# Kernel tuning notes

Hardware: AMD Instinct MI355X
Metric: run time of the kernel (lower is better)

The kernel has to match this reference:

```python
import jax, jax.numpy as jnp
import numpy as np

E = 8          # num_experts
K = 2          # experts_per_token
D = 1024       # d_model
F = 2048       # dim_feedforward
B, S = 2, 2048

def setup_inputs() -> dict:
    key = jax.random.key(0)
    ks = jax.random.split(key, 5)
    scale = 0.02
    return {
        "x":   jax.random.normal(ks[0], (B, S, D), jnp.float32),
        "Wr":  jax.random.normal(ks[1], (E, D), jnp.float32) * scale,
        "temp": jnp.ones((1,), jnp.float32),
        "W1":  jax.random.normal(ks[2], (E, 2 * F, D), jnp.float32) * scale,
        "b1":  jnp.zeros((E, 2 * F), jnp.float32),
        "W2":  jax.random.normal(ks[3], (E, D, F), jnp.float32) * scale,
        "b2":  jnp.zeros((E, D), jnp.float32),
    }

def reference(x, Wr, temp, W1, b1, W2, b2):
    b, s, d = x.shape
    xf = x.reshape(-1, d)                                   # [T, D]
    router_logits = (xf @ Wr.T) / temp                      # [T, E]
    # eval mode: no router noise, dropout is identity
    top_w, top_idx = jax.lax.top_k(router_logits, K)        # [T, K]
    top_w = jax.nn.softmax(top_w, axis=-1)                  # renormalize over top-k
    # dense gate matrix [T, E]: weight if expert selected else 0 (topk indices are distinct)
    gates = jnp.sum(jax.nn.one_hot(top_idx, E, dtype=xf.dtype) * top_w[..., None], axis=1)
    out = jnp.zeros_like(xf)
    for e in range(E):  # fixed small expert loop, dense compute gated to zero for unrouted tokens
        h = xf @ W1[e].T + b1[e]                            # [T, 2F]
        a = h[:, :F] * jax.nn.silu(h[:, F:])                # SwiGLU -> [T, F]
        y = a @ W2[e].T + b2[e]                             # [T, D]
        out = out + y * gates[:, e:e + 1]
    return out.reshape(b, s, d)
```

## Files before the change

### kernel.cpp

```cpp
#include <hip/hip_runtime.h>
#include <hip/hip_bf16.h>

#define DEV __device__ __forceinline__

namespace {

constexpr int D     = 1024;
constexpr int F     = 2048;
constexpr int E     = 8;
constexpr int TWO_F = 2 * F;

typedef short bf16x8 __attribute__((ext_vector_type(8)));
typedef float f32x4  __attribute__((ext_vector_type(4)));

DEV unsigned short f32_to_bf16(float f) {
  unsigned int u = __builtin_bit_cast(unsigned int, f);
  u += 0x7fffu + ((u >> 16) & 1u);
  return (unsigned short)(u >> 16);
}

DEV void load_lds16(const void* g, void* l) {
  __builtin_amdgcn_global_load_lds((const __attribute__((address_space(1))) void*)g,
                                   (__attribute__((address_space(3))) void*)l, 16, 0, 0);
}

DEV const bf16x8* frag_addr(const unsigned short* S, int row, int kk, int quad) {
  int cl = (((kk >> 3) + quad) ^ (row & 7));
  return (const bf16x8*)(S + row * 64 + cl * 8);
}

__global__ void zero_kernel(float* __restrict__ p, int n4) {
  int i = blockIdx.x * 256 + threadIdx.x;
  if (i < n4) ((float4*)p)[i] = make_float4(0.f, 0.f, 0.f, 0.f);
}

__global__ void cvt_all_kernel(const float* __restrict__ x, const float* __restrict__ W1,
                               const float* __restrict__ W2,
                               unsigned short* __restrict__ xb, unsigned short* __restrict__ W1b,
                               unsigned short* __restrict__ W2b,
                               long long nx, long long n1) {
  long long i = (long long)(blockIdx.x * 256 + threadIdx.x) * 8;
  const float* src;
  unsigned short* dst;
  long long off;
  if (i < nx)            { src = x;  dst = xb;  off = i; }
  else if (i < nx + n1)  { src = W1; dst = W1b; off = i - nx; }
  else                   { src = W2; dst = W2b; off = i - nx - n1; }
  float4 a = *(const float4*)(src + off);
  float4 b = *(const float4*)(src + off + 4);
  uint4 o;
  o.x = (unsigned)f32_to_bf16(a.x) | ((unsigned)f32_to_bf16(a.y) << 16);
  o.y = (unsigned)f32_to_bf16(a.z) | ((unsigned)f32_to_bf16(a.w) << 16);
  o.z = (unsigned)f32_to_bf16(b.x) | ((unsigned)f32_to_bf16(b.y) << 16);
  o.w = (unsigned)f32_to_bf16(b.z) | ((unsigned)f32_to_bf16(b.w) << 16);
  *(uint4*)(dst + off) = o;
}

__global__ void router_kernel(const float* __restrict__ x, const float* __restrict__ Wr,
                              const float* __restrict__ temp,
                              int* __restrict__ topk_idx, float* __restrict__ topk_gate, int T) {
  int wid  = blockIdx.x * 4 + (threadIdx.x >> 6);
  int lane = threadIdx.x & 63;
  if (wid >= T) return;
  const float* xr = x + (size_t)wid * D;
  float acc[E];
#pragma unroll
  for (int e = 0; e < E; ++e) acc[e] = 0.f;
  int base = lane * 16;
#pragma unroll
  for (int u = 0; u < 4; ++u) {
    float4 xv = *(const float4*)(xr + base + u * 4);
#pragma unroll
    for (int e = 0; e < E; ++e) {
      float4 wv = *(const float4*)(Wr + e * D + base + u * 4);
      acc[e] += xv.x * wv.x + xv.y * wv.y + xv.z * wv.z + xv.w * wv.w;
    }
  }
#pragma unroll
  for (int e = 0; e < E; ++e) {
    float v = acc[e];
#pragma unroll
    for (int off = 32; off > 0; off >>= 1) v += __shfl_xor(v, off, 64);
    acc[e] = v;
  }
  if (lane == 0) {
    float inv = 1.0f / temp[0];
    float l[E];
#pragma unroll
    for (int e = 0; e < E; ++e) l[e] = acc[e] * inv;
    int e0 = 0;
#pragma unroll
    for (int e = 1; e < E; ++e) if (l[e] > l[e0]) e0 = e;
    int e1 = (e0 == 0) ? 1 : 0;
#pragma unroll
    for (int e = 0; e < E; ++e) if (e != e0 && l[e] > l[e1]) e1 = e;
    float dlt = l[e1] - l[e0];
    float ed  = __expf(dlt);
    topk_idx[2 * wid]      = e0;
    topk_idx[2 * wid + 1]  = e1;
    topk_gate[2 * wid]     = 1.f / (1.f + ed);
    topk_gate[2 * wid + 1] = ed / (1.f + ed);
  }
}

__global__ __launch_bounds__(1024)
void assign_kernel(const int* __restrict__ topk_idx, const float* __restrict__ topk_gate,
                   int* __restrict__ counts, int* __restrict__ offsets,
                   int* __restrict__ row_token, float* __restrict__ row_gate, int T) {
  __shared__ int hist[E];
  __shared__ int cur[E];
  const int tid = threadIdx.x;
  if (tid < E) hist[tid] = 0;
  __syncthreads();
  for (int t = tid; t < T; t += 1024) {
    atomicAdd(&hist[topk_idx[2 * t]], 1);
    atomicAdd(&hist[topk_idx[2 * t + 1]], 1);
  }
  __syncthreads();
  if (tid == 0) {
    int s = 0;
    for (int e = 0; e < E; ++e) {
      int c = hist[e];
      counts[e]  = c;
      offsets[e] = s;
      cur[e]     = s;
      s += c;
    }
  }
  __syncthreads();
  for (int t = tid; t < T; t += 1024) {
#pragma unroll
    for (int s = 0; s < 2; ++s) {
      int e = topk_idx[2 * t + s];
      int p = atomicAdd(&cur[e], 1);
      row_token[p] = t;
      row_gate[p]  = topk_gate[2 * t + s];
    }
  }
}

__global__ __launch_bounds__(256, 2)
void gemm1_kernel(const unsigned short* __restrict__ xb,
                  const unsigned short* __restrict__ W1b,
                  const float* __restrict__ b1,
                  const int* __restrict__ counts, const int* __restrict__ offsets,
                  const int* __restrict__ row_token,
                  unsigned short* __restrict__ a_buf) {
  const int e  = blockIdx.z;
  const int m0 = blockIdx.y * 128;
  const int n0 = blockIdx.x * 64;
  const int cnt = counts[e];
  if (m0 >= cnt) return;
  const int pairBase = offsets[e];

  __shared__ __align__(16) unsigned short As[128 * 64];
  __shared__ __align__(16) unsigned short Bs[128 * 64];
  __shared__ int tokS[128];

  const int tid = threadIdx.x;
  if (tid < 128) {
    int r = m0 + tid;
    tokS[tid] = (r < cnt) ? row_token[pairBase + r] : row_token[pairBase];
  }
  __syncthreads();

  const int lane = tid & 63;
  const int wave = tid >> 6;
  const int quad = lane >> 4;
  const int l16  = lane & 15;
  const int lr   = lane >> 3;
  const int lc   = lane & 7;
  const int sw   = lc ^ (lr & 7);
  const int wr   = wave >> 1;
  const int wc   = wave & 1;

  const unsigned short* W1e = W1b + (size_t)e * TWO_F * D;
  const unsigned short* aptr[4];
  const unsigned short* bptr[4];
#pragma unroll
  for (int i = 0; i < 4; ++i) {
    int r = wave * 32 + i * 8 + lr;
    aptr[i] = xb + (size_t)tokS[r] * D + sw * 8;
    int g = r >> 5, s = r & 31;
    int wrow = (g & 1) * F + n0 + (g >> 1) * 32 + s;
    bptr[i] = W1e + (size_t)wrow * D + sw * 8;
  }
  unsigned short* AsW = As + (wave * 32) * 64;
  unsigned short* BsW = Bs + (wave * 32) * 64;

  f32x4 acc[4][4];
#pragma unroll
  for (int i = 0; i < 4; ++i)
#pragma unroll
    for (int j = 0; j < 4; ++j) acc[i][j] = (f32x4){0.f, 0.f, 0.f, 0.f};

  for (int k0 = 0; k0 < D; k0 += 64) {
#pragma unroll
    for (int i = 0; i < 4; ++i) load_lds16(aptr[i] + k0, AsW + i * 8 * 64);
#pragma unroll
    for (int i = 0; i < 4; ++i) load_lds16(bptr[i] + k0, BsW + i * 8 * 64);
    __syncthreads();
#pragma unroll
    for (int kk = 0; kk < 64; kk += 32) {
      bf16x8 af[4], bf[4];
#pragma unroll
      for (int i = 0; i < 4; ++i)
        af[i] = *frag_addr(As, wr * 64 + i * 16 + l16, kk, quad);
#pragma unroll
      for (int j = 0; j < 4; ++j)
        bf[j] = *frag_addr(Bs, wc * 64 + j * 16 + l16, kk, quad);
#pragma unroll
      for (int i = 0; i < 4; ++i)
#pragma unroll
        for (int j = 0; j < 4; ++j)
          acc[i][j] = __builtin_amdgcn_mfma_f32_16x16x32_bf16(af[i], bf[j], acc[i][j], 0, 0, 0);
    }
    __syncthreads();
  }

#pragma unroll
  for (int i = 0; i < 4; ++i) {
    int rb = wr * 64 + i * 16 + quad * 4;
#pragma unroll
    for (int j = 0; j < 2; ++j) {
      int col = n0 + wc * 32 + j * 16 + l16;
      float bh1 = b1[e * TWO_F + col];
      float bh2 = b1[e * TWO_F + F + col];
#pragma unroll
      for (int rg = 0; rg < 4; ++rg) {
        int r = rb + rg;
        if (m0 + r < cnt) {
          float h1 = acc[i][j][rg] + bh1;
          float h2 = acc[i][j + 2][rg] + bh2;
          float a  = h1 * (h2 / (1.f + __expf(-h2)));
          a_buf[(size_t)(pairBase + m0 + r) * F + col] = f32_to_bf16(a);
        }
      }
    }
  }
}

__global__ __launch_bounds__(256, 2)
void gemm2_kernel(const unsigned short* __restrict__ a_buf,
                  const unsigned short* __restrict__ W2b,
                  const float* __restrict__ b2,
                  const int* __restrict__ counts, const int* __restrict__ offsets,
                  const int* __restrict__ row_token, const float* __restrict__ row_gate,
                  float* __restrict__ out, int totalPairs) {
  const int e  = blockIdx.z;
  const int m0 = blockIdx.y * 128;
  const int n0 = blockIdx.x * 128;
  const int cnt = counts[e];
  if (m0 >= cnt) return;
  const int pairBase = offsets[e];

  __shared__ __align__(16) unsigned short As[128 * 64];
  __shared__ __align__(16) unsigned short Bs[128 * 64];
  __shared__ int   tokS[128];
  __shared__ float gateS[128];

  const int tid = threadIdx.x;
  if (tid < 128) {
    int r = m0 + tid;
    bool v = (r < cnt);
    tokS[tid]  = v ? row_token[pairBase + r] : 0;
    gateS[tid] = v ? row_gate[pairBase + r] : 0.f;
  }
  __syncthreads();

  const int lane = tid & 63;
  const int wave = tid >> 6;
  const int quad = lane >> 4;
  const int l16  = lane & 15;
  const int lr   = lane >> 3;
  const int lc   = lane & 7;
  const int sw   = lc ^ (lr & 7);
  const int wr   = wave >> 1;
  const int wc   = wave & 1;

  const unsigned short* W2e = W2b + (size_t)e * D * F;
  const unsigned short* aptr[4];
  const unsigned short* bptr[4];
#pragma unroll
  for (int i = 0; i < 4; ++i) {
    int r = wave * 32 + i * 8 + lr;
    int g = pairBase + m0 + r;
    if (g > totalPairs - 1) g = totalPairs - 1;
    aptr[i] = a_buf + (size_t)g * F + sw * 8;
    bptr[i] = W2e + (size_t)(n0 + r) * F + sw * 8;
  }
  unsigned short* AsW = As + (wave * 32) * 64;
  unsigned short* BsW = Bs + (wave * 32) * 64;

  f32x4 acc[4][4];
#pragma unroll
  for (int i = 0; i < 4; ++i)
#pragma unroll
    for (int j = 0; j < 4; ++j) acc[i][j] = (f32x4){0.f, 0.f, 0.f, 0.f};

  for (int k0 = 0; k0 < F; k0 += 64) {
#pragma unroll
    for (int i = 0; i < 4; ++i) load_lds16(aptr[i] + k0, AsW + i * 8 * 64);
#pragma unroll
    for (int i = 0; i < 4; ++i) load_lds16(bptr[i] + k0, BsW + i * 8 * 64);
    __syncthreads();
#pragma unroll
    for (int kk = 0; kk < 64; kk += 32) {
      bf16x8 af[4], bf[4];
#pragma unroll
      for (int i = 0; i < 4; ++i)
        af[i] = *frag_addr(As, wr * 64 + i * 16 + l16, kk, quad);
#pragma unroll
      for (int j = 0; j < 4; ++j)
        bf[j] = *frag_addr(Bs, wc * 64 + j * 16 + l16, kk, quad);
#pragma unroll
      for (int i = 0; i < 4; ++i)
#pragma unroll
        for (int j = 0; j < 4; ++j)
          acc[i][j] = __builtin_amdgcn_mfma_f32_16x16x32_bf16(af[i], bf[j], acc[i][j], 0, 0, 0);
    }
    __syncthreads();
  }

#pragma unroll
  for (int j = 0; j < 4; ++j) {
    int col = n0 + wc * 64 + j * 16 + l16;
    float b2v = b2[e * D + col];
#pragma unroll
    for (int i = 0; i < 4; ++i) {
      int rb = wr * 64 + i * 16 + quad * 4;
#pragma unroll
      for (int rg = 0; rg < 4; ++rg) {
        int r = rb + rg;
        if (m0 + r < cnt) {
          float y = (acc[i][j][rg] + b2v) * gateS[r];
          atomicAdd(&out[(size_t)tokS[r] * D + col], y);
        }
      }
    }
  }
}

}

extern "C" void kernel_launch(void* const* d_in, const int* in_sizes, int n_in,
                              void* d_out, int out_size, void* d_ws, size_t ws_size,
                              hipStream_t stream) {
  (void)n_in; (void)out_size; (void)ws_size;
  const float* x    = (const float*)d_in[0];
  const float* Wr   = (const float*)d_in[1];
  const float* temp = (const float*)d_in[2];
  const float* W1   = (const float*)d_in[3];
  const float* b1   = (const float*)d_in[4];
  const float* W2   = (const float*)d_in[5];
  const float* b2   = (const float*)d_in[6];
  float* out = (float*)d_out;
  const int T = in_sizes[0] / D;

  char* ws = (char*)d_ws;
  size_t off = 0;
  unsigned short* xb    = (unsigned short*)(ws + off); off += (size_t)T * D * 2;
  unsigned short* W1b   = (unsigned short*)(ws + off); off += (size_t)E * TWO_F * D * 2;
  unsigned short* W2b   = (unsigned short*)(ws + off); off += (size_t)E * D * F * 2;
  unsigned short* a_buf = (unsigned short*)(ws + off); off += (size_t)T * 2 * F * 2;
  int*   counts    = (int*)(ws + off); off += 64;
  int*   offsets   = (int*)(ws + off); off += 64;
  int*   topk_idx  = (int*)(ws + off); off += (size_t)T * 2 * 4;
  float* topk_gate = (float*)(ws + off); off += (size_t)T * 2 * 4;
  int*   row_token = (int*)(ws + off); off += (size_t)T * 2 * 4;
  float* row_gate  = (float*)(ws + off); off += (size_t)T * 2 * 4;

  const long long nx = (long long)T * D;
  const long long n1 = (long long)E * TWO_F * D;
  const long long n2 = (long long)E * D * F;

  zero_kernel<<<(T * D / 4 + 255) / 256, 256, 0, stream>>>(out, T * D / 4);
  router_kernel<<<(T + 3) / 4, 256, 0, stream>>>(x, Wr, temp, topk_idx, topk_gate, T);
  assign_kernel<<<1, 1024, 0, stream>>>(topk_idx, topk_gate, counts, offsets,
                                        row_token, row_gate, T);
  cvt_all_kernel<<<(int)((nx + n1 + n2) / 2048), 256, 0, stream>>>(x, W1, W2, xb, W1b, W2b,
                                                                   nx, n1);
  gemm1_kernel<<<dim3(F / 64, (T * 2 + 127) / 128, E), 256, 0, stream>>>(xb, W1b, b1, counts,
                                                                         offsets, row_token, a_buf);
  gemm2_kernel<<<dim3(D / 128, (T * 2 + 127) / 128, E), 256, 0, stream>>>(a_buf, W2b, b2, counts,
                                                                          offsets, row_token,
                                                                          row_gate, out, T * 2);
}
```

Measured before the change: 476.6 us.

## Replace atomic scatter-add with bf16 expert output buffer and gather combine

Removes the zero kernel and the float atomicAdd scatter in gemm2. gemm2 now writes bf16 per-pair outputs into a buffer that reuses the W1b workspace, and a new combine kernel gathers each token's two expert rows and applies the gate weights. The assign kernel now uses deterministic ballot/popcount ranking instead of shared atomics and records each pair's position. Launch bounds on both GEMMs are raised to 4 blocks per CU. Costs are an extra launch, an extra bf16 round trip for expert outputs, and possible register pressure from the higher occupancy target.

```diff
diff --git a/kernel.cpp b/kernel.cpp
--- a/kernel.cpp
+++ b/kernel.cpp
@@ -19,6 +19,11 @@
   return (unsigned short)(u >> 16);
 }
 
+DEV float bf16_to_f32(unsigned short h) {
+  unsigned int u = ((unsigned int)h) << 16;
+  return __builtin_bit_cast(float, u);
+}
+
 DEV void load_lds16(const void* g, void* l) {
   __builtin_amdgcn_global_load_lds((const __attribute__((address_space(1))) void*)g,
                                    (__attribute__((address_space(3))) void*)l, 16, 0, 0);
@@ -27,11 +32,6 @@
 DEV const bf16x8* frag_addr(const unsigned short* S, int row, int kk, int quad) {
   int cl = (((kk >> 3) + quad) ^ (row & 7));
   return (const bf16x8*)(S + row * 64 + cl * 8);
-}
-
-__global__ void zero_kernel(float* __restrict__ p, int n4) {
-  int i = blockIdx.x * 256 + threadIdx.x;
-  if (i < n4) ((float4*)p)[i] = make_float4(0.f, 0.f, 0.f, 0.f);
 }
 
 __global__ void cvt_all_kernel(const float* __restrict__ x, const float* __restrict__ W1,
@@ -105,41 +105,65 @@
 
 __global__ __launch_bounds__(1024)
 void assign_kernel(const int* __restrict__ topk_idx, const float* __restrict__ topk_gate,
-                   int* __restrict__ counts, int* __restrict__ offsets,
-                   int* __restrict__ row_token, float* __restrict__ row_gate, int T) {
-  __shared__ int hist[E];
-  __shared__ int cur[E];
-  const int tid = threadIdx.x;
-  if (tid < E) hist[tid] = 0;
+                   int* __restrict__ counts, int* __restrict__ offsets_g,
+                   int* __restrict__ row_token, float* __restrict__ row_gate,
+                   int* __restrict__ pos, int T) {
+  __shared__ int cntS[128 * E];
+  __shared__ int baseS[128 * E];
+  __shared__ int totS[E];
+  __shared__ int offS[E];
+  const int tid  = threadIdx.x;
+  const int w    = tid >> 6;
+  const int lane = tid & 63;
+  const int Q    = 2 * T;
+  const unsigned long long lm = (1ull << lane) - 1ull;
+
+  int eReg[8], rReg[8];
+#pragma unroll
+  for (int c = 0; c < 8; ++c) {
+    int q = (w * 8 + c) * 64 + lane;
+    int e = (q < Q) ? topk_idx[q] : -1;
+    eReg[c] = e;
+    int r = 0;
+#pragma unroll
+    for (int ee = 0; ee < E; ++ee) {
+      unsigned long long m = __ballot(e == ee);
+      if (lane == ee) cntS[(w * 8 + c) * E + ee] = __popcll(m);
+      if (e == ee) r = __popcll(m & lm);
+    }
+    rReg[c] = r;
+  }
   __syncthreads();
-  for (int t = tid; t < T; t += 1024) {
-    atomicAdd(&hist[topk_idx[2 * t]], 1);
-    atomicAdd(&hist[topk_idx[2 * t + 1]], 1);
+  if (tid < E) {
+    int s = 0;
+    for (int k = 0; k < 128; ++k) { baseS[k * E + tid] = s; s += cntS[k * E + tid]; }
+    totS[tid] = s;
   }
   __syncthreads();
   if (tid == 0) {
     int s = 0;
     for (int e = 0; e < E; ++e) {
-      int c = hist[e];
-      counts[e]  = c;
-      offsets[e] = s;
-      cur[e]     = s;
-      s += c;
+      offS[e] = s;
+      counts[e] = totS[e];
+      offsets_g[e] = s;
+      s += totS[e];
     }
   }
   __syncthreads();
-  for (int t = tid; t < T; t += 1024) {
-#pragma unroll
-    for (int s = 0; s < 2; ++s) {
-      int e = topk_idx[2 * t + s];
-      int p = atomicAdd(&cur[e], 1);
-      row_token[p] = t;
-      row_gate[p]  = topk_gate[2 * t + s];
-    }
-  }
-}
-
-__global__ __launch_bounds__(256, 2)
+#pragma unroll
+  for (int c = 0; c < 8; ++c) {
+    int q = (w * 8 + c) * 64 + lane;
+    if (q < Q) {
+      int e = eReg[c];
+      int p = offS[e] + baseS[(w * 8 + c) * E + e] + rReg[c];
+      row_token[p] = q >> 1;
+      row_gate[p]  = topk_gate[q];
+      pos[q]       = p;
+    }
+  }
+}
+
+__global__ __launch_bounds__(256, 4)
 void gemm1_kernel(const unsigned short* __restrict__ xb,
                   const unsigned short* __restrict__ W1b,
                   const float* __restrict__ b1,
@@ -240,13 +264,12 @@
   }
 }
 
-__global__ __launch_bounds__(256, 2)
+__global__ __launch_bounds__(256, 4)
 void gemm2_kernel(const unsigned short* __restrict__ a_buf,
                   const unsigned short* __restrict__ W2b,
                   const float* __restrict__ b2,
                   const int* __restrict__ counts, const int* __restrict__ offsets,
-                  const int* __restrict__ row_token, const float* __restrict__ row_gate,
-                  float* __restrict__ out, int totalPairs) {
+                  unsigned short* __restrict__ y_buf, int totalPairs) {
   const int e  = blockIdx.z;
   const int m0 = blockIdx.y * 128;
   const int n0 = blockIdx.x * 128;
@@ -256,18 +279,8 @@
 
   __shared__ __align__(16) unsigned short As[128 * 64];
   __shared__ __align__(16) unsigned short Bs[128 * 64];
-  __shared__ int   tokS[128];
-  __shared__ float gateS[128];
-
-  const int tid = threadIdx.x;
-  if (tid < 128) {
-    int r = m0 + tid;
-    bool v = (r < cnt);
-    tokS[tid]  = v ? row_token[pairBase + r] : 0;
-    gateS[tid] = v ? row_gate[pairBase + r] : 0.f;
-  }
-  __syncthreads();
-
+
+  const int tid  = threadIdx.x;
   const int lane = tid & 63;
   const int wave = tid >> 6;
   const int quad = lane >> 4;
@@ -332,13 +345,29 @@
 #pragma unroll
       for (int rg = 0; rg < 4; ++rg) {
         int r = rb + rg;
-        if (m0 + r < cnt) {
-          float y = (acc[i][j][rg] + b2v) * gateS[r];
-          atomicAdd(&out[(size_t)tokS[r] * D + col], y);
-        }
+        if (m0 + r < cnt)
+          y_buf[(size_t)(pairBase + m0 + r) * D + col] = f32_to_bf16(acc[i][j][rg] + b2v);
       }
     }
   }
+}
+
+__global__ void combine_kernel(const unsigned short* __restrict__ y_buf,
+                               const int* __restrict__ pos,
+                               const float* __restrict__ topk_gate,
+                               float* __restrict__ out) {
+  const int t = blockIdx.x;
+  const int d = threadIdx.x * 4;
+  const int p0 = pos[2 * t], p1 = pos[2 * t + 1];
+  const float g0 = topk_gate[2 * t], g1 = topk_gate[2 * t + 1];
+  ushort4 a = *(const ushort4*)(y_buf + (size_t)p0 * D + d);
+  ushort4 b = *(const ushort4*)(y_buf + (size_t)p1 * D + d);
+  float4 o;
+  o.x = g0 * bf16_to_f32(a.x) + g1 * bf16_to_f32(b.x);
+  o.y = g0 * bf16_to_f32(a.y) + g1 * bf16_to_f32(b.y);
+  o.z = g0 * bf16_to_f32(a.z) + g1 * bf16_to_f32(b.z);
+  o.w = g0 * bf16_to_f32(a.w) + g1 * bf16_to_f32(b.w);
+  *(float4*)(out + (size_t)t * D + d) = o;
 }
 
 }
@@ -369,20 +398,21 @@
   float* topk_gate = (float*)(ws + off); off += (size_t)T * 2 * 4;
   int*   row_token = (int*)(ws + off); off += (size_t)T * 2 * 4;
   float* row_gate  = (float*)(ws + off); off += (size_t)T * 2 * 4;
+  int*   pos       = (int*)(ws + off); off += (size_t)T * 2 * 4;
+  unsigned short* y_buf = W1b;
 
   const long long nx = (long long)T * D;
   const long long n1 = (long long)E * TWO_F * D;
   const long long n2 = (long long)E * D * F;
 
-  zero_kernel<<<(T * D / 4 + 255) / 256, 256, 0, stream>>>(out, T * D / 4);
   router_kernel<<<(T + 3) / 4, 256, 0, stream>>>(x, Wr, temp, topk_idx, topk_gate, T);
   assign_kernel<<<1, 1024, 0, stream>>>(topk_idx, topk_gate, counts, offsets,
-                                        row_token, row_gate, T);
+                                        row_token, row_gate, pos, T);
   cvt_all_kernel<<<(int)((nx + n1 + n2) / 2048), 256, 0, stream>>>(x, W1, W2, xb, W1b, W2b,
                                                                    nx, n1);
   gemm1_kernel<<<dim3(F / 64, (T * 2 + 127) / 128, E), 256, 0, stream>>>(xb, W1b, b1, counts,
                                                                          offsets, row_token, a_buf);
   gemm2_kernel<<<dim3(D / 128, (T * 2 + 127) / 128, E), 256, 0, stream>>>(a_buf, W2b, b2, counts,
-                                                                          offsets, row_token,
-                                                                          row_gate, out, T * 2);
-}
+                                                                          offsets, y_buf, T * 2);
+  combine_kernel<<<T, 256, 0, stream>>>(y_buf, pos, topk_gate, out);
+}
```

Result: slower. 581.3 us (+22.0%).
